# Kernel tuning notes

Measured on AMD Instinct MI355X. Metric: run time of the kernel, lower is better.

The kernel has to match this reference:

```python
import jax, jax.numpy as jnp
import numpy as np

D_MODEL = 512
DK = 4
DV = 8
HIDD = 10
HEAD = D_MODEL // DV  # 64
LN_EPS = 1e-5


def setup_inputs() -> dict:
    key = jax.random.key(0)
    ks = jax.random.split(key, 10)
    B, S, Se = 8, 512, 512
    u = jax.random.uniform  # torch.rand initializer for attention weights
    n = jax.random.normal
    return {
        "x": n(ks[0], (B, S, D_MODEL), jnp.float32),
        "x_enc": n(ks[1], (B, Se, D_MODEL), jnp.float32),
        "WqM": u(ks[2], (D_MODEL, HEAD * DK), jnp.float32),
        "WkM": u(ks[3], (D_MODEL, HEAD * DK), jnp.float32),
        "WvM": u(ks[4], (D_MODEL, HEAD * DV), jnp.float32),
        "ln_g": jnp.ones((D_MODEL,), jnp.float32),
        "ln_b": jnp.zeros((D_MODEL,), jnp.float32),
        "fc1_w": n(ks[5], (HIDD, D_MODEL), jnp.float32) * (1.0 / np.sqrt(D_MODEL)),
        "fc1_b": jnp.zeros((HIDD,), jnp.float32),
        "fc2_w": n(ks[6], (D_MODEL, HIDD), jnp.float32) * (1.0 / np.sqrt(HIDD)),
        "fc2_b": jnp.zeros((D_MODEL,), jnp.float32),
    }


def _attention(Xq, Xkv, WqM, WkM, WvM, causal_mul_mask):
    # NOTE: cross-attention in the source also uses WqM/WkM/WvM (Wq/Wk/Wv unused).
    B, Sq, _ = Xq.shape
    Sk = Xkv.shape[1]
    Q = (Xq @ WqM).reshape(B, Sq, HEAD, DK)
    K = (Xkv @ WkM).reshape(B, Sk, HEAD, DK)
    V = (Xkv @ WvM).reshape(B, Sk, HEAD, DV)
    score = jnp.einsum('bqhd,bkhd->bhqk', Q, K) / np.sqrt(DK).astype(np.float32)
    if causal_mul_mask:
        # Faithful quirk: multiplicative tril mask on scores (NOT additive -inf).
        score = score * jnp.tril(jnp.ones((Sq, Sk), score.dtype))
    w = jax.nn.softmax(score, axis=-1)
    out = jnp.einsum('bhqk,bkhd->bqhd', w, V)
    return out.reshape(B, Sq, HEAD * DV)  # HEAD*DV == d_model


def _layernorm(x, g, b):
    mu = jnp.mean(x, axis=-1, keepdims=True)
    var = jnp.mean(jnp.square(x - mu), axis=-1, keepdims=True)
    return (x - mu) * jax.lax.rsqrt(var + LN_EPS) * g + b


def reference(x, x_enc, WqM, WkM, WvM, ln_g, ln_b, fc1_w, fc1_b, fc2_w, fc2_b):
    fx = _attention(x, x, WqM, WkM, WvM, causal_mul_mask=True)
    fx = _attention(fx, x_enc, WqM, WkM, WvM, causal_mul_mask=False)
    y = _layernorm(x + fx, ln_g, ln_b)
    h = jax.nn.relu(y @ fc1_w.T + fc1_b)
    return h @ fc2_w.T + fc2_b
```

## Files before the change

### kernel.cpp

```cpp
#include <hip/hip_runtime.h>
#include <math.h>

#define D_MODEL 512
#define BATCH 8
#define SEQ 512
#define HEAD 64
#define DK 4
#define DV 8
#define HIDD 10

#define MR 64
#define KC 32
#define NC 256

__global__ __launch_bounds__(256) void proj_kernel(
    const float* __restrict__ xq, const float* __restrict__ xkv,
    const float* __restrict__ Wq, const float* __restrict__ Wk,
    const float* __restrict__ Wv,
    float* __restrict__ Q2, float* __restrict__ K2, float* __restrict__ V2)
{
    __shared__ float xt[KC * MR];
    __shared__ float wt[KC * NC];

    const int t  = threadIdx.x;
    const int bj = blockIdx.x & 3;
    const int br = blockIdx.x >> 2;
    const int r0 = br * MR;

    const float* X; const float* W; int ldw; int c0;
    if (bj == 0)      { X = xq;  W = Wq; ldw = 256; c0 = 0;   }
    else if (bj == 1) { X = xkv; W = Wk; ldw = 256; c0 = 0;   }
    else if (bj == 2) { X = xkv; W = Wv; ldw = 512; c0 = 0;   }
    else              { X = xkv; W = Wv; ldw = 512; c0 = 256; }

    const int ct = t & 31;
    const int rt = t >> 5;
    const int rs = t & 63;
    const int kx = t >> 6;
    const int rg = t >> 6;
    const int cq = t & 63;

    float acc[8][8];
#pragma unroll
    for (int r = 0; r < 8; ++r)
#pragma unroll
        for (int c = 0; c < 8; ++c) acc[r][c] = 0.f;

    for (int kc = 0; kc < D_MODEL; kc += KC) {
        {
            const float4 xa = *(const float4*)(X + (long)(r0 + rs) * D_MODEL + kc + kx * 8);
            const float4 xb = *(const float4*)(X + (long)(r0 + rs) * D_MODEL + kc + kx * 8 + 4);
            xt[(kx * 8 + 0) * MR + rs] = xa.x;
            xt[(kx * 8 + 1) * MR + rs] = xa.y;
            xt[(kx * 8 + 2) * MR + rs] = xa.z;
            xt[(kx * 8 + 3) * MR + rs] = xa.w;
            xt[(kx * 8 + 4) * MR + rs] = xb.x;
            xt[(kx * 8 + 5) * MR + rs] = xb.y;
            xt[(kx * 8 + 6) * MR + rs] = xb.z;
            xt[(kx * 8 + 7) * MR + rs] = xb.w;
        }
#pragma unroll
        for (int i = 0; i < 8; ++i) {
            const int row = i * 4 + rg;
            *(float4*)(wt + row * NC + cq * 4) =
                *(const float4*)(W + (long)(kc + row) * ldw + c0 + cq * 4);
        }
        __syncthreads();

#pragma unroll 2
        for (int k = 0; k < KC; ++k) {
            const float4 w0 = *(const float4*)(wt + k * NC + ct * 8);
            const float4 w1 = *(const float4*)(wt + k * NC + ct * 8 + 4);
            const float4 x0 = *(const float4*)(xt + k * MR + rt * 8);
            const float4 x1 = *(const float4*)(xt + k * MR + rt * 8 + 4);
            const float xr[8] = {x0.x, x0.y, x0.z, x0.w, x1.x, x1.y, x1.z, x1.w};
            const float wc[8] = {w0.x, w0.y, w0.z, w0.w, w1.x, w1.y, w1.z, w1.w};
#pragma unroll
            for (int r = 0; r < 8; ++r)
#pragma unroll
                for (int c = 0; c < 8; ++c)
                    acc[r][c] = fmaf(xr[r], wc[c], acc[r][c]);
        }
        __syncthreads();
    }

    const int b  = r0 >> 9;
    const int sb = (r0 & 511) + rt * 8;
    if (bj <= 1) {
        float* dst = (bj == 0) ? Q2 : K2;
        const long h0 = (long)b * HEAD + ct * 2;
#pragma unroll
        for (int r = 0; r < 8; ++r) {
            *(float4*)(dst + (h0 * SEQ + sb + r) * 4) =
                make_float4(acc[r][0], acc[r][1], acc[r][2], acc[r][3]);
            *(float4*)(dst + ((h0 + 1) * SEQ + sb + r) * 4) =
                make_float4(acc[r][4], acc[r][5], acc[r][6], acc[r][7]);
        }
    } else {
        const int h = (c0 >> 3) + ct;
        const long vb = ((long)b * HEAD + h) * SEQ;
#pragma unroll
        for (int r = 0; r < 8; ++r) {
            *(float4*)(V2 + (vb + sb + r) * 8) =
                make_float4(acc[r][0], acc[r][1], acc[r][2], acc[r][3]);
            *(float4*)(V2 + (vb + sb + r) * 8 + 4) =
                make_float4(acc[r][4], acc[r][5], acc[r][6], acc[r][7]);
        }
    }
}

template <int CAUSAL>
__global__ __launch_bounds__(256) void attn_kernel(
    const float* __restrict__ Q2, const float* __restrict__ K2,
    const float* __restrict__ V2, float* __restrict__ O)
{
    extern __shared__ float smem[];
    float* Kl = smem;
    float* Vl = smem + SEQ * DK;
    float* cs = Vl + SEQ * DV;

    const int t = threadIdx.x;
    const int bh = blockIdx.x;
    const int b = bh >> 6;
    const int h = bh & 63;

    const float4* Ks = (const float4*)(K2 + (long)bh * SEQ * DK);
    ((float4*)Kl)[t]       = Ks[t];
    ((float4*)Kl)[t + 256] = Ks[t + 256];
    const float4* Vs = (const float4*)(V2 + (long)bh * SEQ * DV);
#pragma unroll
    for (int i = 0; i < 4; ++i)
        ((float4*)Vl)[t + i * 256] = Vs[t + i * 256];
    __syncthreads();

    if (CAUSAL) {
        const int ch = t >> 3, d = t & 7;
        float s16 = 0.f;
#pragma unroll
        for (int i = 0; i < 16; ++i) s16 += Vl[(ch * 16 + i) * 8 + d];
        cs[ch * 8 + d] = s16;
        __syncthreads();
        if (t < 8) {
            cs[256 + t] = 0.f;
            float run = 0.f;
            for (int c2 = 31; c2 >= 0; --c2) {
                run += cs[c2 * 8 + t];
                cs[c2 * 8 + t] = run;
            }
        }
        __syncthreads();
    }

    const int q0 = 2 * t, q1 = 2 * t + 1;
    const float4 qa = *(const float4*)(Q2 + ((long)bh * SEQ + q0) * 4);
    const float4 qb = *(const float4*)(Q2 + ((long)bh * SEQ + q1) * 4);
    const float qa0 = qa.x*0.5f, qa1 = qa.y*0.5f, qa2 = qa.z*0.5f, qa3 = qa.w*0.5f;
    const float qb0 = qb.x*0.5f, qb1 = qb.y*0.5f, qb2 = qb.z*0.5f, qb3 = qb.w*0.5f;

    const int bound = CAUSAL ? q1 : (SEQ - 1);

    float m0 = -INFINITY, l0 = 0.f, m1 = -INFINITY, l1 = 0.f;
    float A0[8], A1[8];
#pragma unroll
    for (int d = 0; d < 8; ++d) { A0[d] = 0.f; A1[d] = 0.f; }

    int s0 = 0;
    for (; s0 + 8 <= bound + 1; s0 += 8) {
        float sa[8], sb[8];
#pragma unroll
        for (int i = 0; i < 8; ++i) {
            const float4 k4 = *(const float4*)(Kl + (s0 + i) * 4);
            sa[i] = fmaf(qa0, k4.x, fmaf(qa1, k4.y, fmaf(qa2, k4.z, qa3 * k4.w)));
            sb[i] = fmaf(qb0, k4.x, fmaf(qb1, k4.y, fmaf(qb2, k4.z, qb3 * k4.w)));
            if (CAUSAL) sa[i] = (s0 + i <= q0) ? sa[i] : 0.f;
        }
        float ga = fmaxf(fmaxf(fmaxf(sa[0], sa[1]), fmaxf(sa[2], sa[3])),
                         fmaxf(fmaxf(sa[4], sa[5]), fmaxf(sa[6], sa[7])));
        float gb = fmaxf(fmaxf(fmaxf(sb[0], sb[1]), fmaxf(sb[2], sb[3])),
                         fmaxf(fmaxf(sb[4], sb[5]), fmaxf(sb[6], sb[7])));
        if (ga > m0) {
            float sc = __expf(m0 - ga);
            l0 *= sc;
#pragma unroll
            for (int d = 0; d < 8; ++d) A0[d] *= sc;
            m0 = ga;
        }
        if (gb > m1) {
            float sc = __expf(m1 - gb);
            l1 *= sc;
#pragma unroll
            for (int d = 0; d < 8; ++d) A1[d] *= sc;
            m1 = gb;
        }
#pragma unroll
        for (int i = 0; i < 8; ++i) {
            float p0 = __expf(sa[i] - m0);
            float p1 = __expf(sb[i] - m1);
            l0 += p0; l1 += p1;
            const float4 v0 = *(const float4*)(Vl + (s0 + i) * 8);
            const float4 v1 = *(const float4*)(Vl + (s0 + i) * 8 + 4);
            A0[0] = fmaf(p0, v0.x, A0[0]); A0[1] = fmaf(p0, v0.y, A0[1]);
            A0[2] = fmaf(p0, v0.z, A0[2]); A0[3] = fmaf(p0, v0.w, A0[3]);
            A0[4] = fmaf(p0, v1.x, A0[4]); A0[5] = fmaf(p0, v1.y, A0[5]);
            A0[6] = fmaf(p0, v1.z, A0[6]); A0[7] = fmaf(p0, v1.w, A0[7]);
            A1[0] = fmaf(p1, v0.x, A1[0]); A1[1] = fmaf(p1, v0.y, A1[1]);
            A1[2] = fmaf(p1, v0.z, A1[2]); A1[3] = fmaf(p1, v0.w, A1[3]);
            A1[4] = fmaf(p1, v1.x, A1[4]); A1[5] = fmaf(p1, v1.y, A1[5]);
            A1[6] = fmaf(p1, v1.z, A1[6]); A1[7] = fmaf(p1, v1.w, A1[7]);
        }
    }
    for (int s = s0; s <= bound; ++s) {
        const float4 k4 = *(const float4*)(Kl + s * 4);
        float sa = fmaf(qa0, k4.x, fmaf(qa1, k4.y, fmaf(qa2, k4.z, qa3 * k4.w)));
        float sb = fmaf(qb0, k4.x, fmaf(qb1, k4.y, fmaf(qb2, k4.z, qb3 * k4.w)));
        if (CAUSAL) sa = (s <= q0) ? sa : 0.f;
        if (sa > m0) {
            float sc = __expf(m0 - sa);
            l0 *= sc;
#pragma unroll
            for (int d = 0; d < 8; ++d) A0[d] *= sc;
            m0 = sa;
        }
        if (sb > m1) {
            float sc = __expf(m1 - sb);
            l1 *= sc;
#pragma unroll
            for (int d = 0; d < 8; ++d) A1[d] *= sc;
            m1 = sb;
        }
        float p0 = __expf(sa - m0);
        float p1 = __expf(sb - m1);
        l0 += p0; l1 += p1;
        const float4 v0 = *(const float4*)(Vl + s * 8);
        const float4 v1 = *(const float4*)(Vl + s * 8 + 4);
        A0[0] = fmaf(p0, v0.x, A0[0]); A0[1] = fmaf(p0, v0.y, A0[1]);
        A0[2] = fmaf(p0, v0.z, A0[2]); A0[3] = fmaf(p0, v0.w, A0[3]);
        A0[4] = fmaf(p0, v1.x, A0[4]); A0[5] = fmaf(p0, v1.y, A0[5]);
        A0[6] = fmaf(p0, v1.z, A0[6]); A0[7] = fmaf(p0, v1.w, A0[7]);
        A1[0] = fmaf(p1, v0.x, A1[0]); A1[1] = fmaf(p1, v0.y, A1[1]);
        A1[2] = fmaf(p1, v0.z, A1[2]); A1[3] = fmaf(p1, v0.w, A1[3]);
        A1[4] = fmaf(p1, v1.x, A1[4]); A1[5] = fmaf(p1, v1.y, A1[5]);
        A1[6] = fmaf(p1, v1.z, A1[6]); A1[7] = fmaf(p1, v1.w, A1[7]);
    }

    if (CAUSAL && t < 255) {
        const int n = SEQ - 1 - q1;
        const int nq = q1 + 1;
        const int cq2 = nq >> 4;
        float sv[8];
#pragma unroll
        for (int d = 0; d < 8; ++d) sv[d] = cs[(cq2 + 1) * 8 + d];
        for (int s = nq; s < (cq2 + 1) * 16; ++s) {
            const float4 v0 = *(const float4*)(Vl + s * 8);
            const float4 v1 = *(const float4*)(Vl + s * 8 + 4);
            sv[0]+=v0.x; sv[1]+=v0.y; sv[2]+=v0.z; sv[3]+=v0.w;
            sv[4]+=v1.x; sv[5]+=v1.y; sv[6]+=v1.z; sv[7]+=v1.w;
        }
        float pm0 = __expf(-m0);
        l0 += pm0 * (float)n;
#pragma unroll
        for (int d = 0; d < 8; ++d) A0[d] = fmaf(pm0, sv[d], A0[d]);

        float M1 = fmaxf(m1, 0.f);
        float sc1 = __expf(m1 - M1);
        float pm1 = __expf(-M1);
        l1 = l1 * sc1 + pm1 * (float)n;
#pragma unroll
        for (int d = 0; d < 8; ++d) A1[d] = A1[d] * sc1 + pm1 * sv[d];
    }

    const float i0 = 1.0f / l0, i1 = 1.0f / l1;
    const long ob0 = ((long)b * SEQ + q0) * 512 + h * DV;
    const long ob1 = ((long)b * SEQ + q1) * 512 + h * DV;
    *(float4*)(O + ob0)     = make_float4(A0[0]*i0, A0[1]*i0, A0[2]*i0, A0[3]*i0);
    *(float4*)(O + ob0 + 4) = make_float4(A0[4]*i0, A0[5]*i0, A0[6]*i0, A0[7]*i0);
    *(float4*)(O + ob1)     = make_float4(A1[0]*i1, A1[1]*i1, A1[2]*i1, A1[3]*i1);
    *(float4*)(O + ob1 + 4) = make_float4(A1[4]*i1, A1[5]*i1, A1[6]*i1, A1[7]*i1);
}

__global__ __launch_bounds__(256) void ln_mlp_kernel(
    const float* __restrict__ x, const float* __restrict__ fx,
    const float* __restrict__ g, const float* __restrict__ beta,
    const float* __restrict__ w1, const float* __restrict__ b1,
    const float* __restrict__ w2, const float* __restrict__ b2,
    float* __restrict__ out)
{
    const int t = threadIdx.x;
    const int lane = t & 63;
    const int row = blockIdx.x * 4 + (t >> 6);
    const long base = (long)row * D_MODEL;
    const int e0 = lane * 8;

    const float4 xa = *(const float4*)(x + base + e0);
    const float4 xb = *(const float4*)(x + base + e0 + 4);
    const float4 fa = *(const float4*)(fx + base + e0);
    const float4 fb = *(const float4*)(fx + base + e0 + 4);
    float z[8] = {xa.x+fa.x, xa.y+fa.y, xa.z+fa.z, xa.w+fa.w,
                  xb.x+fb.x, xb.y+fb.y, xb.z+fb.z, xb.w+fb.w};

    float sum = 0.f;
#pragma unroll
    for (int j = 0; j < 8; ++j) sum += z[j];
#pragma unroll
    for (int o = 32; o > 0; o >>= 1) sum += __shfl_xor(sum, o);
    float mu = sum * (1.0f / 512.0f);

    float d[8], ss = 0.f;
#pragma unroll
    for (int j = 0; j < 8; ++j) { d[j] = z[j] - mu; ss += d[j] * d[j]; }
#pragma unroll
    for (int o = 32; o > 0; o >>= 1) ss += __shfl_xor(ss, o);
    float rs = rsqrtf(ss * (1.0f / 512.0f) + 1e-5f);

    const float4 ga = *(const float4*)(g + e0);
    const float4 gb = *(const float4*)(g + e0 + 4);
    const float4 ba = *(const float4*)(beta + e0);
    const float4 bb = *(const float4*)(beta + e0 + 4);
    const float gg[8] = {ga.x,ga.y,ga.z,ga.w,gb.x,gb.y,gb.z,gb.w};
    const float bt[8] = {ba.x,ba.y,ba.z,ba.w,bb.x,bb.y,bb.z,bb.w};
    float y[8];
#pragma unroll
    for (int j = 0; j < 8; ++j) y[j] = d[j] * rs * gg[j] + bt[j];

    float part[HIDD];
#pragma unroll
    for (int i = 0; i < HIDD; ++i) {
        const float4 wa = *(const float4*)(w1 + i * 512 + e0);
        const float4 wb = *(const float4*)(w1 + i * 512 + e0 + 4);
        part[i] = y[0]*wa.x + y[1]*wa.y + y[2]*wa.z + y[3]*wa.w
                + y[4]*wb.x + y[5]*wb.y + y[6]*wb.z + y[7]*wb.w;
    }
#pragma unroll
    for (int i = 0; i < HIDD; ++i)
#pragma unroll
        for (int o = 32; o > 0; o >>= 1) part[i] += __shfl_xor(part[i], o);

    float hv[HIDD];
#pragma unroll
    for (int i = 0; i < HIDD; ++i) hv[i] = fmaxf(part[i] + b1[i], 0.f);

    float o8[8];
#pragma unroll
    for (int j = 0; j < 8; ++j) o8[j] = b2[e0 + j];
#pragma unroll
    for (int i = 0; i < HIDD; ++i)
#pragma unroll
        for (int j = 0; j < 8; ++j)
            o8[j] = fmaf(hv[i], w2[(long)(e0 + j) * 10 + i], o8[j]);

    *(float4*)(out + base + e0)     = make_float4(o8[0], o8[1], o8[2], o8[3]);
    *(float4*)(out + base + e0 + 4) = make_float4(o8[4], o8[5], o8[6], o8[7]);
}

extern "C" void kernel_launch(void* const* d_in, const int* in_sizes, int n_in,
                              void* d_out, int out_size, void* d_ws, size_t ws_size,
                              hipStream_t stream) {
    (void)in_sizes; (void)n_in; (void)out_size; (void)ws_size;
    const float* x    = (const float*)d_in[0];
    const float* xenc = (const float*)d_in[1];
    const float* Wq   = (const float*)d_in[2];
    const float* Wk   = (const float*)d_in[3];
    const float* Wv   = (const float*)d_in[4];
    const float* ln_g = (const float*)d_in[5];
    const float* ln_b = (const float*)d_in[6];
    const float* w1   = (const float*)d_in[7];
    const float* b1   = (const float*)d_in[8];
    const float* w2   = (const float*)d_in[9];
    const float* b2   = (const float*)d_in[10];
    float* out = (float*)d_out;

    float* ws = (float*)d_ws;
    float* Q2 = ws;
    float* K2 = Q2 + 1048576;
    float* V2 = K2 + 1048576;
    float* A  = V2 + 2097152;

    const int nrows = BATCH * SEQ;
    const size_t lds_cross  = (size_t)(SEQ * DK + SEQ * DV) * 4;
    const size_t lds_causal = lds_cross + (size_t)(33 * DV) * 4;
    const int proj_grid = (nrows / MR) * 4;

    proj_kernel<<<dim3(proj_grid), 256, 0, stream>>>(x, x, Wq, Wk, Wv, Q2, K2, V2);
    attn_kernel<1><<<dim3(BATCH * HEAD), 256, lds_causal, stream>>>(Q2, K2, V2, A);

    proj_kernel<<<dim3(proj_grid), 256, 0, stream>>>(A, xenc, Wq, Wk, Wv, Q2, K2, V2);
    attn_kernel<0><<<dim3(BATCH * HEAD), 256, lds_cross, stream>>>(Q2, K2, V2, A);

    ln_mlp_kernel<<<dim3(nrows / 4), 256, 0, stream>>>(x, A, ln_g, ln_b,
                                                       w1, b1, w2, b2, out);
}
```

Baseline: 403.6 us.

## Split-K projection into two partial buffers and split attention queries across blocks

The projection kernel gains a split-K mode: each block handles half the reduction dimension and writes a partial Q/K/V to a separate workspace set, which doubles the grid. The attention kernel sums the two partials while loading into LDS. Attention blocks now use 128 threads, each covering half of the query rows, so the attention grid doubles as well. Column mapping in the projection is changed to contiguous float4 chunks. The aim is better occupancy on many CUs, at the cost of extra global traffic for the partials and recomputing the K/V loads and causal prefix sums in every block.

```diff
diff --git a/kernel.cpp b/kernel.cpp
--- a/kernel.cpp
+++ b/kernel.cpp
@@ -13,19 +13,25 @@
 #define KC 32
 #define NC 256
 
+template <int SPLIT>
 __global__ __launch_bounds__(256) void proj_kernel(
     const float* __restrict__ xq, const float* __restrict__ xkv,
     const float* __restrict__ Wq, const float* __restrict__ Wk,
     const float* __restrict__ Wv,
-    float* __restrict__ Q2, float* __restrict__ K2, float* __restrict__ V2)
+    float* __restrict__ Qa, float* __restrict__ Ka, float* __restrict__ Va,
+    float* __restrict__ Qb, float* __restrict__ Kb, float* __restrict__ Vb)
 {
     __shared__ float xt[KC * MR];
     __shared__ float wt[KC * NC];
 
-    const int t  = threadIdx.x;
-    const int bj = blockIdx.x & 3;
-    const int br = blockIdx.x >> 2;
-    const int r0 = br * MR;
+    const int t   = threadIdx.x;
+    const int bid = blockIdx.x;
+    const int ks  = SPLIT ? (bid & 1) : 0;
+    const int bj  = SPLIT ? ((bid >> 1) & 3) : (bid & 3);
+    const int br  = SPLIT ? (bid >> 3) : (bid >> 2);
+    const int r0  = br * MR;
+    const int kbase = ks * 256;
+    const int kend  = kbase + (SPLIT ? 256 : 512);
 
     const float* X; const float* W; int ldw; int c0;
     if (bj == 0)      { X = xq;  W = Wq; ldw = 256; c0 = 0;   }
@@ -33,53 +39,64 @@
     else if (bj == 2) { X = xkv; W = Wv; ldw = 512; c0 = 0;   }
     else              { X = xkv; W = Wv; ldw = 512; c0 = 256; }
 
-    const int ct = t & 31;
-    const int rt = t >> 5;
-    const int rs = t & 63;
-    const int kx = t >> 6;
-    const int rg = t >> 6;
-    const int cq = t & 63;
-
-    float acc[8][8];
-#pragma unroll
-    for (int r = 0; r < 8; ++r)
-#pragma unroll
-        for (int c = 0; c < 8; ++c) acc[r][c] = 0.f;
-
-    for (int kc = 0; kc < D_MODEL; kc += KC) {
+    float* Q2 = ks ? Qb : Qa;
+    float* K2 = ks ? Kb : Ka;
+    float* V2 = ks ? Vb : Va;
+
+    const int ct   = t & 31;
+    const int rt   = t >> 5;
+    const int rs   = t & 63;
+    const int kx   = t >> 6;
+    const int lane = t & 63;
+    const int wv   = t >> 6;
+
+    float4 accL[8], accH[8];
+#pragma unroll
+    for (int r = 0; r < 8; ++r) {
+        accL[r] = make_float4(0.f, 0.f, 0.f, 0.f);
+        accH[r] = make_float4(0.f, 0.f, 0.f, 0.f);
+    }
+
+    for (int kc = kbase; kc < kend; kc += KC) {
         {
-            const float4 xa = *(const float4*)(X + (long)(r0 + rs) * D_MODEL + kc + kx * 8);
-            const float4 xb = *(const float4*)(X + (long)(r0 + rs) * D_MODEL + kc + kx * 8 + 4);
-            xt[(kx * 8 + 0) * MR + rs] = xa.x;
-            xt[(kx * 8 + 1) * MR + rs] = xa.y;
-            xt[(kx * 8 + 2) * MR + rs] = xa.z;
-            xt[(kx * 8 + 3) * MR + rs] = xa.w;
-            xt[(kx * 8 + 4) * MR + rs] = xb.x;
-            xt[(kx * 8 + 5) * MR + rs] = xb.y;
-            xt[(kx * 8 + 6) * MR + rs] = xb.z;
-            xt[(kx * 8 + 7) * MR + rs] = xb.w;
+            const float* xb = X + (long)(r0 + rs) * D_MODEL + kc + kx * 8;
+            const float4 xa4 = *(const float4*)(xb);
+            const float4 xb4 = *(const float4*)(xb + 4);
+            xt[(kx * 8 + 0) * MR + rs] = xa4.x;
+            xt[(kx * 8 + 1) * MR + rs] = xa4.y;
+            xt[(kx * 8 + 2) * MR + rs] = xa4.z;
+            xt[(kx * 8 + 3) * MR + rs] = xa4.w;
+            xt[(kx * 8 + 4) * MR + rs] = xb4.x;
+            xt[(kx * 8 + 5) * MR + rs] = xb4.y;
+            xt[(kx * 8 + 6) * MR + rs] = xb4.z;
+            xt[(kx * 8 + 7) * MR + rs] = xb4.w;
         }
 #pragma unroll
         for (int i = 0; i < 8; ++i) {
-            const int row = i * 4 + rg;
-            *(float4*)(wt + row * NC + cq * 4) =
-                *(const float4*)(W + (long)(kc + row) * ldw + c0 + cq * 4);
+            const int row = i * 4 + wv;
+            *(float4*)(wt + row * NC + lane * 4) =
+                *(const float4*)(W + (long)(kc + row) * ldw + c0 + lane * 4);
         }
         __syncthreads();
 
 #pragma unroll 2
         for (int k = 0; k < KC; ++k) {
-            const float4 w0 = *(const float4*)(wt + k * NC + ct * 8);
-            const float4 w1 = *(const float4*)(wt + k * NC + ct * 8 + 4);
+            const float4 w0 = *(const float4*)(wt + k * NC + ct * 4);
+            const float4 w1 = *(const float4*)(wt + k * NC + 128 + ct * 4);
             const float4 x0 = *(const float4*)(xt + k * MR + rt * 8);
             const float4 x1 = *(const float4*)(xt + k * MR + rt * 8 + 4);
             const float xr[8] = {x0.x, x0.y, x0.z, x0.w, x1.x, x1.y, x1.z, x1.w};
-            const float wc[8] = {w0.x, w0.y, w0.z, w0.w, w1.x, w1.y, w1.z, w1.w};
-#pragma unroll
-            for (int r = 0; r < 8; ++r)
-#pragma unroll
-                for (int c = 0; c < 8; ++c)
-                    acc[r][c] = fmaf(xr[r], wc[c], acc[r][c]);
+#pragma unroll
+            for (int r = 0; r < 8; ++r) {
+                accL[r].x = fmaf(xr[r], w0.x, accL[r].x);
+                accL[r].y = fmaf(xr[r], w0.y, accL[r].y);
+                accL[r].z = fmaf(xr[r], w0.z, accL[r].z);
+                accL[r].w = fmaf(xr[r], w0.w, accL[r].w);
+                accH[r].x = fmaf(xr[r], w1.x, accH[r].x);
+                accH[r].y = fmaf(xr[r], w1.y, accH[r].y);
+                accH[r].z = fmaf(xr[r], w1.z, accH[r].z);
+                accH[r].w = fmaf(xr[r], w1.w, accH[r].w);
+            }
         }
         __syncthreads();
     }
@@ -88,57 +105,78 @@
     const int sb = (r0 & 511) + rt * 8;
     if (bj <= 1) {
         float* dst = (bj == 0) ? Q2 : K2;
-        const long h0 = (long)b * HEAD + ct * 2;
+        const long hlo = ((long)b * HEAD + ct) * SEQ;
+        const long hhi = ((long)b * HEAD + 32 + ct) * SEQ;
 #pragma unroll
         for (int r = 0; r < 8; ++r) {
-            *(float4*)(dst + (h0 * SEQ + sb + r) * 4) =
-                make_float4(acc[r][0], acc[r][1], acc[r][2], acc[r][3]);
-            *(float4*)(dst + ((h0 + 1) * SEQ + sb + r) * 4) =
-                make_float4(acc[r][4], acc[r][5], acc[r][6], acc[r][7]);
+            *(float4*)(dst + (hlo + sb + r) * 4) = accL[r];
+            *(float4*)(dst + (hhi + sb + r) * 4) = accH[r];
         }
     } else {
-        const int h = (c0 >> 3) + ct;
-        const long vb = ((long)b * HEAD + h) * SEQ;
+        const int clo = c0 + ct * 4;
+        const int chi = clo + 128;
+        const long vlo = ((long)b * HEAD + (clo >> 3)) * SEQ;
+        const long vhi = ((long)b * HEAD + (chi >> 3)) * SEQ;
+        const int off = (ct & 1) * 4;
 #pragma unroll
         for (int r = 0; r < 8; ++r) {
-            *(float4*)(V2 + (vb + sb + r) * 8) =
-                make_float4(acc[r][0], acc[r][1], acc[r][2], acc[r][3]);
-            *(float4*)(V2 + (vb + sb + r) * 8 + 4) =
-                make_float4(acc[r][4], acc[r][5], acc[r][6], acc[r][7]);
+            *(float4*)(V2 + (vlo + sb + r) * 8 + off) = accL[r];
+            *(float4*)(V2 + (vhi + sb + r) * 8 + off) = accH[r];
         }
     }
 }
 
-template <int CAUSAL>
-__global__ __launch_bounds__(256) void attn_kernel(
-    const float* __restrict__ Q2, const float* __restrict__ K2,
-    const float* __restrict__ V2, float* __restrict__ O)
+template <int CAUSAL, int ADD2>
+__global__ __launch_bounds__(128) void attn_kernel(
+    const float* __restrict__ Qa, const float* __restrict__ Ka,
+    const float* __restrict__ Va, const float* __restrict__ Qb,
+    const float* __restrict__ Kb, const float* __restrict__ Vb,
+    float* __restrict__ O)
 {
     extern __shared__ float smem[];
     float* Kl = smem;
     float* Vl = smem + SEQ * DK;
     float* cs = Vl + SEQ * DV;
 
-    const int t = threadIdx.x;
-    const int bh = blockIdx.x;
-    const int b = bh >> 6;
-    const int h = bh & 63;
-
-    const float4* Ks = (const float4*)(K2 + (long)bh * SEQ * DK);
-    ((float4*)Kl)[t]       = Ks[t];
-    ((float4*)Kl)[t + 256] = Ks[t + 256];
-    const float4* Vs = (const float4*)(V2 + (long)bh * SEQ * DV);
-#pragma unroll
-    for (int i = 0; i < 4; ++i)
-        ((float4*)Vl)[t + i * 256] = Vs[t + i * 256];
+    const int t  = threadIdx.x;
+    const int qh = blockIdx.x & 1;
+    const int bh = blockIdx.x >> 1;
+    const int b  = bh >> 6;
+    const int h  = bh & 63;
+
+    const float4* Ksa = (const float4*)(Ka + (long)bh * SEQ * DK);
+    const float4* Ksb = (const float4*)(Kb + (long)bh * SEQ * DK);
+#pragma unroll
+    for (int i = 0; i < 4; ++i) {
+        float4 v = Ksa[t + i * 128];
+        if (ADD2) {
+            const float4 w = Ksb[t + i * 128];
+            v.x += w.x; v.y += w.y; v.z += w.z; v.w += w.w;
+        }
+        ((float4*)Kl)[t + i * 128] = v;
+    }
+    const float4* Vsa = (const float4*)(Va + (long)bh * SEQ * DV);
+    const float4* Vsb = (const float4*)(Vb + (long)bh * SEQ * DV);
+#pragma unroll
+    for (int i = 0; i < 8; ++i) {
+        float4 v = Vsa[t + i * 128];
+        if (ADD2) {
+            const float4 w = Vsb[t + i * 128];
+            v.x += w.x; v.y += w.y; v.z += w.z; v.w += w.w;
+        }
+        ((float4*)Vl)[t + i * 128] = v;
+    }
     __syncthreads();
 
     if (CAUSAL) {
-        const int ch = t >> 3, d = t & 7;
-        float s16 = 0.f;
-#pragma unroll
-        for (int i = 0; i < 16; ++i) s16 += Vl[(ch * 16 + i) * 8 + d];
-        cs[ch * 8 + d] = s16;
+#pragma unroll
+        for (int w = t; w < 256; w += 128) {
+            const int ch = w >> 3, d = w & 7;
+            float s16 = 0.f;
+#pragma unroll
+            for (int i = 0; i < 16; ++i) s16 += Vl[(ch * 16 + i) * 8 + d];
+            cs[ch * 8 + d] = s16;
+        }
         __syncthreads();
         if (t < 8) {
             cs[256 + t] = 0.f;
@@ -151,51 +189,56 @@
         __syncthreads();
     }
 
-    const int q0 = 2 * t, q1 = 2 * t + 1;
-    const float4 qa = *(const float4*)(Q2 + ((long)bh * SEQ + q0) * 4);
-    const float4 qb = *(const float4*)(Q2 + ((long)bh * SEQ + q1) * 4);
-    const float qa0 = qa.x*0.5f, qa1 = qa.y*0.5f, qa2 = qa.z*0.5f, qa3 = qa.w*0.5f;
-    const float qb0 = qb.x*0.5f, qb1 = qb.y*0.5f, qb2 = qb.z*0.5f, qb3 = qb.w*0.5f;
-
-    const int bound = CAUSAL ? q1 : (SEQ - 1);
+    const int q0 = qh * 256 + 2 * t, q1 = q0 + 1;
+    float4 qva = *(const float4*)(Qa + ((long)bh * SEQ + q0) * 4);
+    float4 qvb = *(const float4*)(Qa + ((long)bh * SEQ + q1) * 4);
+    if (ADD2) {
+        const float4 wa = *(const float4*)(Qb + ((long)bh * SEQ + q0) * 4);
+        const float4 wb = *(const float4*)(Qb + ((long)bh * SEQ + q1) * 4);
+        qva.x += wa.x; qva.y += wa.y; qva.z += wa.z; qva.w += wa.w;
+        qvb.x += wb.x; qvb.y += wb.y; qvb.z += wb.z; qvb.w += wb.w;
+    }
+    const float qa0 = qva.x*0.5f, qa1 = qva.y*0.5f, qa2 = qva.z*0.5f, qa3 = qva.w*0.5f;
+    const float qb0 = qvb.x*0.5f, qb1 = qvb.y*0.5f, qb2 = qvb.z*0.5f, qb3 = qvb.w*0.5f;
 
     float m0 = -INFINITY, l0 = 0.f, m1 = -INFINITY, l1 = 0.f;
     float A0[8], A1[8];
 #pragma unroll
     for (int d = 0; d < 8; ++d) { A0[d] = 0.f; A1[d] = 0.f; }
 
+    const int full_end = CAUSAL ? (q0 + 1) : SEQ;
+
     int s0 = 0;
-    for (; s0 + 8 <= bound + 1; s0 += 8) {
+    for (; s0 + 8 <= full_end; s0 += 8) {
         float sa[8], sb[8];
 #pragma unroll
         for (int i = 0; i < 8; ++i) {
             const float4 k4 = *(const float4*)(Kl + (s0 + i) * 4);
             sa[i] = fmaf(qa0, k4.x, fmaf(qa1, k4.y, fmaf(qa2, k4.z, qa3 * k4.w)));
             sb[i] = fmaf(qb0, k4.x, fmaf(qb1, k4.y, fmaf(qb2, k4.z, qb3 * k4.w)));
-            if (CAUSAL) sa[i] = (s0 + i <= q0) ? sa[i] : 0.f;
-        }
-        float ga = fmaxf(fmaxf(fmaxf(sa[0], sa[1]), fmaxf(sa[2], sa[3])),
-                         fmaxf(fmaxf(sa[4], sa[5]), fmaxf(sa[6], sa[7])));
-        float gb = fmaxf(fmaxf(fmaxf(sb[0], sb[1]), fmaxf(sb[2], sb[3])),
-                         fmaxf(fmaxf(sb[4], sb[5]), fmaxf(sb[6], sb[7])));
+        }
+        const float ga = fmaxf(fmaxf(fmaxf(sa[0], sa[1]), fmaxf(sa[2], sa[3])),
+                               fmaxf(fmaxf(sa[4], sa[5]), fmaxf(sa[6], sa[7])));
+        const float gb = fmaxf(fmaxf(fmaxf(sb[0], sb[1]), fmaxf(sb[2], sb[3])),
+                               fmaxf(fmaxf(sb[4], sb[5]), fmaxf(sb[6], sb[7])));
         if (ga > m0) {
-            float sc = __expf(m0 - ga);
-            l0 *= sc;
-#pragma unroll
-            for (int d = 0; d < 8; ++d) A0[d] *= sc;
+            const float r = __expf(m0 - ga);
+            l0 *= r;
+#pragma unroll
+            for (int d = 0; d < 8; ++d) A0[d] *= r;
             m0 = ga;
         }
         if (gb > m1) {
-            float sc = __expf(m1 - gb);
-            l1 *= sc;
-#pragma unroll
-            for (int d = 0; d < 8; ++d) A1[d] *= sc;
+            const float r = __expf(m1 - gb);
+            l1 *= r;
+#pragma unroll
+            for (int d = 0; d < 8; ++d) A1[d] *= r;
             m1 = gb;
         }
 #pragma unroll
         for (int i = 0; i < 8; ++i) {
-            float p0 = __expf(sa[i] - m0);
-            float p1 = __expf(sb[i] - m1);
+            const float p0 = __expf(sa[i] - m0);
+            const float p1 = __expf(sb[i] - m1);
             l0 += p0; l1 += p1;
             const float4 v0 = *(const float4*)(Vl + (s0 + i) * 8);
             const float4 v1 = *(const float4*)(Vl + (s0 + i) * 8 + 4);
@@ -209,64 +252,67 @@
             A1[6] = fmaf(p1, v1.z, A1[6]); A1[7] = fmaf(p1, v1.w, A1[7]);
         }
     }
-    for (int s = s0; s <= bound; ++s) {
-        const float4 k4 = *(const float4*)(Kl + s * 4);
-        float sa = fmaf(qa0, k4.x, fmaf(qa1, k4.y, fmaf(qa2, k4.z, qa3 * k4.w)));
-        float sb = fmaf(qb0, k4.x, fmaf(qb1, k4.y, fmaf(qb2, k4.z, qb3 * k4.w)));
-        if (CAUSAL) sa = (s <= q0) ? sa : 0.f;
-        if (sa > m0) {
-            float sc = __expf(m0 - sa);
-            l0 *= sc;
-#pragma unroll
-            for (int d = 0; d < 8; ++d) A0[d] *= sc;
-            m0 = sa;
-        }
-        if (sb > m1) {
-            float sc = __expf(m1 - sb);
-            l1 *= sc;
-#pragma unroll
-            for (int d = 0; d < 8; ++d) A1[d] *= sc;
-            m1 = sb;
-        }
-        float p0 = __expf(sa - m0);
-        float p1 = __expf(sb - m1);
-        l0 += p0; l1 += p1;
-        const float4 v0 = *(const float4*)(Vl + s * 8);
-        const float4 v1 = *(const float4*)(Vl + s * 8 + 4);
-        A0[0] = fmaf(p0, v0.x, A0[0]); A0[1] = fmaf(p0, v0.y, A0[1]);
-        A0[2] = fmaf(p0, v0.z, A0[2]); A0[3] = fmaf(p0, v0.w, A0[3]);
-        A0[4] = fmaf(p0, v1.x, A0[4]); A0[5] = fmaf(p0, v1.y, A0[5]);
-        A0[6] = fmaf(p0, v1.z, A0[6]); A0[7] = fmaf(p0, v1.w, A0[7]);
-        A1[0] = fmaf(p1, v0.x, A1[0]); A1[1] = fmaf(p1, v0.y, A1[1]);
-        A1[2] = fmaf(p1, v0.z, A1[2]); A1[3] = fmaf(p1, v0.w, A1[3]);
-        A1[4] = fmaf(p1, v1.x, A1[4]); A1[5] = fmaf(p1, v1.y, A1[5]);
-        A1[6] = fmaf(p1, v1.z, A1[6]); A1[7] = fmaf(p1, v1.w, A1[7]);
-    }
-
-    if (CAUSAL && t < 255) {
-        const int n = SEQ - 1 - q1;
-        const int nq = q1 + 1;
-        const int cq2 = nq >> 4;
-        float sv[8];
-#pragma unroll
-        for (int d = 0; d < 8; ++d) sv[d] = cs[(cq2 + 1) * 8 + d];
-        for (int s = nq; s < (cq2 + 1) * 16; ++s) {
+
+    if (CAUSAL) {
+        for (int s = s0; s <= q1; ++s) {
+            const float4 k4 = *(const float4*)(Kl + s * 4);
+            float sa = fmaf(qa0, k4.x, fmaf(qa1, k4.y, fmaf(qa2, k4.z, qa3 * k4.w)));
+            float sb = fmaf(qb0, k4.x, fmaf(qb1, k4.y, fmaf(qb2, k4.z, qb3 * k4.w)));
+            sa = (s <= q0) ? sa : 0.f;
+            if (sa > m0) {
+                const float r = __expf(m0 - sa);
+                l0 *= r;
+#pragma unroll
+                for (int d = 0; d < 8; ++d) A0[d] *= r;
+                m0 = sa;
+            }
+            if (sb > m1) {
+                const float r = __expf(m1 - sb);
+                l1 *= r;
+#pragma unroll
+                for (int d = 0; d < 8; ++d) A1[d] *= r;
+                m1 = sb;
+            }
+            const float p0 = __expf(sa - m0);
+            const float p1 = __expf(sb - m1);
+            l0 += p0; l1 += p1;
             const float4 v0 = *(const float4*)(Vl + s * 8);
             const float4 v1 = *(const float4*)(Vl + s * 8 + 4);
-            sv[0]+=v0.x; sv[1]+=v0.y; sv[2]+=v0.z; sv[3]+=v0.w;
-            sv[4]+=v1.x; sv[5]+=v1.y; sv[6]+=v1.z; sv[7]+=v1.w;
-        }
-        float pm0 = __expf(-m0);
-        l0 += pm0 * (float)n;
-#pragma unroll
-        for (int d = 0; d < 8; ++d) A0[d] = fmaf(pm0, sv[d], A0[d]);
-
-        float M1 = fmaxf(m1, 0.f);
-        float sc1 = __expf(m1 - M1);
-        float pm1 = __expf(-M1);
-        l1 = l1 * sc1 + pm1 * (float)n;
-#pragma unroll
-        for (int d = 0; d < 8; ++d) A1[d] = A1[d] * sc1 + pm1 * sv[d];
+            A0[0] = fmaf(p0, v0.x, A0[0]); A0[1] = fmaf(p0, v0.y, A0[1]);
+            A0[2] = fmaf(p0, v0.z, A0[2]); A0[3] = fmaf(p0, v0.w, A0[3]);
+            A0[4] = fmaf(p0, v1.x, A0[4]); A0[5] = fmaf(p0, v1.y, A0[5]);
+            A0[6] = fmaf(p0, v1.z, A0[6]); A0[7] = fmaf(p0, v1.w, A0[7]);
+            A1[0] = fmaf(p1, v0.x, A1[0]); A1[1] = fmaf(p1, v0.y, A1[1]);
+            A1[2] = fmaf(p1, v0.z, A1[2]); A1[3] = fmaf(p1, v0.w, A1[3]);
+            A1[4] = fmaf(p1, v1.x, A1[4]); A1[5] = fmaf(p1, v1.y, A1[5]);
+            A1[6] = fmaf(p1, v1.z, A1[6]); A1[7] = fmaf(p1, v1.w, A1[7]);
+        }
+
+        const int n = SEQ - 1 - q1;
+        if (n > 0) {
+            const int nq  = q1 + 1;
+            const int cq2 = nq >> 4;
+            float sv[8];
+#pragma unroll
+            for (int d = 0; d < 8; ++d) sv[d] = cs[(cq2 + 1) * 8 + d];
+            for (int s = nq; s < (cq2 + 1) * 16; ++s) {
+                const float4 v0 = *(const float4*)(Vl + s * 8);
+                const float4 v1 = *(const float4*)(Vl + s * 8 + 4);
+                sv[0] += v0.x; sv[1] += v0.y; sv[2] += v0.z; sv[3] += v0.w;
+                sv[4] += v1.x; sv[5] += v1.y; sv[6] += v1.z; sv[7] += v1.w;
+            }
+            const float pm0 = __expf(-m0);
+            l0 += pm0 * (float)n;
+#pragma unroll
+            for (int d = 0; d < 8; ++d) A0[d] = fmaf(pm0, sv[d], A0[d]);
+
+            const float M1  = fmaxf(m1, 0.f);
+            const float r1  = __expf(m1 - M1);
+            const float pm1 = __expf(-M1);
+            l1 = l1 * r1 + pm1 * (float)n;
+#pragma unroll
+            for (int d = 0; d < 8; ++d) A1[d] = A1[d] * r1 + pm1 * sv[d];
+        }
     }
 
     const float i0 = 1.0f / l0, i1 = 1.0f / l1;
@@ -355,7 +401,7 @@
 extern "C" void kernel_launch(void* const* d_in, const int* in_sizes, int n_in,
                               void* d_out, int out_size, void* d_ws, size_t ws_size,
                               hipStream_t stream) {
-    (void)in_sizes; (void)n_in; (void)out_size; (void)ws_size;
+    (void)in_sizes; (void)n_in; (void)out_size;
     const float* x    = (const float*)d_in[0];
     const float* xenc = (const float*)d_in[1];
     const float* Wq   = (const float*)d_in[2];
@@ -370,22 +416,39 @@
     float* out = (float*)d_out;
 
     float* ws = (float*)d_ws;
-    float* Q2 = ws;
-    float* K2 = Q2 + 1048576;
-    float* V2 = K2 + 1048576;
-    float* A  = V2 + 2097152;
-
-    const int nrows = BATCH * SEQ;
+    float* Qa = ws;
+    float* Ka = Qa + 1048576;
+    float* Va = Ka + 1048576;
+    const size_t setf = 1048576 + 1048576 + 2097152;
+    const bool split = ws_size >= (size_t)(2 * setf + 2097152) * 4;
+    float* Qb = split ? (Va + 2097152) : Qa;
+    float* Kb = split ? (Qb + 1048576) : Ka;
+    float* Vb = split ? (Kb + 1048576) : Va;
+    float* A  = (split ? (Vb + 2097152) : (Va + 2097152));
+
     const size_t lds_cross  = (size_t)(SEQ * DK + SEQ * DV) * 4;
     const size_t lds_causal = lds_cross + (size_t)(33 * DV) * 4;
-    const int proj_grid = (nrows / MR) * 4;
-
-    proj_kernel<<<dim3(proj_grid), 256, 0, stream>>>(x, x, Wq, Wk, Wv, Q2, K2, V2);
-    attn_kernel<1><<<dim3(BATCH * HEAD), 256, lds_causal, stream>>>(Q2, K2, V2, A);
-
-    proj_kernel<<<dim3(proj_grid), 256, 0, stream>>>(A, xenc, Wq, Wk, Wv, Q2, K2, V2);
-    attn_kernel<0><<<dim3(BATCH * HEAD), 256, lds_cross, stream>>>(Q2, K2, V2, A);
-
-    ln_mlp_kernel<<<dim3(nrows / 4), 256, 0, stream>>>(x, A, ln_g, ln_b,
-                                                       w1, b1, w2, b2, out);
+
+    if (split) {
+        proj_kernel<1><<<dim3(512), 256, 0, stream>>>(x, x, Wq, Wk, Wv,
+                                                      Qa, Ka, Va, Qb, Kb, Vb);
+        attn_kernel<1,1><<<dim3(BATCH * HEAD * 2), 128, lds_causal, stream>>>(
+            Qa, Ka, Va, Qb, Kb, Vb, A);
+        proj_kernel<1><<<dim3(512), 256, 0, stream>>>(A, xenc, Wq, Wk, Wv,
+                                                      Qa, Ka, Va, Qb, Kb, Vb);
+        attn_kernel<0,1><<<dim3(BATCH * HEAD * 2), 128, lds_cross, stream>>>(
+            Qa, Ka, Va, Qb, Kb, Vb, A);
+    } else {
+        proj_kernel<0><<<dim3(256), 256, 0, stream>>>(x, x, Wq, Wk, Wv,
+                                                      Qa, Ka, Va, Qb, Kb, Vb);
+        attn_kernel<1,0><<<dim3(BATCH * HEAD * 2), 128, lds_causal, stream>>>(
+            Qa, Ka, Va, Qb, Kb, Vb, A);
+        proj_kernel<0><<<dim3(256), 256, 0, stream>>>(A, xenc, Wq, Wk, Wv,
+                                                      Qa, Ka, Va, Qb, Kb, Vb);
+        attn_kernel<0,0><<<dim3(BATCH * HEAD * 2), 128, lds_cross, stream>>>(
+            Qa, Ka, Va, Qb, Kb, Vb, A);
+    }
+
+    ln_mlp_kernel<<<dim3(BATCH * SEQ / 4), 256, 0, stream>>>(x, A, ln_g, ln_b,
+                                                             w1, b1, w2, b2, out);
 }
```

New measurement: 349.4 us. -13.4%, faster.
